# Kernel tuning notes

Hardware: AMD Instinct MI355X
Metric: run time of the kernel (lower is better)

## Reference

```python
import jax, jax.numpy as jnp
import numpy as np

V = 50257
VPAD = 50304
D = 768
H = 6
HD = 128
L = 12
T = 2048
BLOCK = 128
NB = T // BLOCK
EPS = 1.1920929e-07  # torch.finfo(float32).eps, F.rms_norm default
ATTN_SCALE = 0.12


def rms_norm(x):
    return x * jax.lax.rsqrt(jnp.mean(jnp.square(x), axis=-1, keepdims=True) + EPS)


def rotary_tables(t):
    af = (1.0 / 1024) ** jnp.linspace(0.0, 1.0, HD // 4)
    af = jnp.concatenate([af, jnp.zeros(HD // 4)])  # half of HD/2 freqs are zero
    theta = jnp.arange(t, dtype=jnp.float32)[:, None] * af[None, :]  # [T, HD/2]
    return jnp.cos(theta), jnp.sin(theta)


def apply_rotary(x, cos, sin):
    # x: [B,T,H,HD]
    x1, x2 = jnp.split(x, 2, axis=-1)
    c = cos[None, :, None, :]
    s = sin[None, :, None, :]
    return jnp.concatenate([x1 * c + x2 * s, -x1 * s + x2 * c], axis=-1)


def build_elem_masks(input_seq, sw_long):
    # Reproduces create_block_masks: block-sparse document-causal + sliding window.
    docs = jnp.cumsum((input_seq == 50256).astype(jnp.int32))
    bi = jnp.arange(NB)
    docs_b = docs.reshape(NB, BLOCK)
    dlo, dhi = docs_b[:, 0], docs_b[:, -1]
    any_bm = (bi[:, None] >= bi[None, :]) & (dlo[:, None] <= dhi[None, :]) & (dhi[:, None] >= dlo[None, :])
    all_bm = (bi[:, None] > bi[None, :]) & (dlo[:, None] == dhi[None, :]) & (dhi[:, None] == dlo[None, :])
    partial_bm = any_bm & (~all_bm)

    def rank_desc(m):
        # rank of each True block among that row's True blocks ordered by descending kv index
        mi = m.astype(jnp.int32)
        return jnp.cumsum(mi[:, ::-1], axis=1)[:, ::-1] - mi

    pr = rank_desc(partial_bm)
    fr = rank_desc(all_bm)
    full_cnt = jnp.sum(all_bm.astype(jnp.int32), axis=1)
    ti = jnp.arange(T)
    causal_e = ti[:, None] >= ti[None, :]
    doc_e = docs[:, None] == docs[None, :]

    def bm(sw):
        # BlockMask.from_kv_blocks keeps nearest blocks:
        # partial kept count = min(partial_cnt, max(sw - full_cnt, 1)); full kept count = min(full_cnt, sw - 1)
        keep_p = partial_bm & (pr < jnp.maximum(sw - full_cnt, 1)[:, None])
        keep_f = all_bm & (fr < (sw - 1))
        kp = jnp.repeat(jnp.repeat(keep_p, BLOCK, axis=0), BLOCK, axis=1)
        kf = jnp.repeat(jnp.repeat(keep_f, BLOCK, axis=0), BLOCK, axis=1)
        # full blocks skip mask_mod; partial blocks apply elementwise document_causal
        return kf | (kp & causal_e & doc_e)

    return bm(sw_long), bm(sw_long // 2)


def attention(x, ve, qkv_w, lam, proj_w, cos, sin, mask):
    B = x.shape[0]
    qkv = jnp.einsum('btd,fd->btf', x, qkv_w.reshape(3 * H * HD, D))
    q, k, v = [a.reshape(B, T, H, HD) for a in jnp.split(qkv, 3, axis=-1)]
    q = apply_rotary(rms_norm(q), cos, sin)
    k = apply_rotary(rms_norm(k), cos, sin)
    if ve is not None:
        v = lam[0] * v + lam[1] * ve.reshape(v.shape)
    else:
        v = lam[0] * v
    scores = jnp.einsum('bthd,bshd->bhts', q, k) * ATTN_SCALE
    scores = jnp.where(mask[None, None], scores, -jnp.inf)
    p = jax.nn.softmax(scores, axis=-1)
    y = jnp.einsum('bhts,bshd->bthd', p, v).reshape(B, T, H * HD)
    return y @ proj_w.T


def mlp(x, fc_w, proj_w):
    h = x @ fc_w.T
    return jnp.square(jax.nn.relu(h)) @ proj_w.T


def forward(input_seq, target_seq, sw, embed_w, ve_w, qkv_w, attn_lambdas, attn_proj_w,
            mlp_fc_w, mlp_proj_w, block_lambdas, skip_weights, lm_head_w):
    long_m, short_m = build_elem_masks(input_seq, sw)
    cos, sin = rotary_tables(T)
    x = x0 = rms_norm(embed_w[input_seq][None])  # [1,T,D]
    ve0, ve1, ve2 = ve_w[0][input_seq], ve_w[1][input_seq], ve_w[2][input_seq]
    ve = [ve0, ve1, ve2, None, None, None, None, None, None, ve0, ve1, ve2]
    enc_masks = [long_m, short_m, short_m, short_m, long_m, short_m]
    masks = enc_masks + enc_masks[::-1]
    skips = []
    for i in range(6):  # encoder
        x = block_lambdas[i, 0] * x + block_lambdas[i, 1] * x0
        x = x + attention(rms_norm(x), ve[i], qkv_w[i], attn_lambdas[i], attn_proj_w[i], cos, sin, masks[i])
        x = x + mlp(rms_norm(x), mlp_fc_w[i], mlp_proj_w[i])
        skips.append(x)
    for j in range(6):  # decoder with U-net skips
        i = 6 + j
        x = x + skip_weights[j] * skips.pop()
        x = block_lambdas[i, 0] * x + block_lambdas[i, 1] * x0
        if i != 7:  # layer 7 has no attention
            x = x + attention(rms_norm(x), ve[i], qkv_w[i], attn_lambdas[i], attn_proj_w[i], cos, sin, masks[i])
        x = x + mlp(rms_norm(x), mlp_fc_w[i], mlp_proj_w[i])
    x = rms_norm(x)
    logits = (x @ lm_head_w.T).astype(jnp.float32)
    logits = 30.0 * jax.nn.sigmoid(logits / (7.5 * (D ** 0.5)))
    logp = jax.nn.log_softmax(logits.reshape(T, VPAD), axis=-1)
    return -jnp.mean(jnp.take_along_axis(logp, target_seq[:, None], axis=1))


def setup_inputs():
    key = jax.random.key(0)
    ks = jax.random.split(key, 10)

    def rn(k, shape, std):
        return jax.random.normal(k, shape, dtype=jnp.float32) * std

    s_d = 0.5 / (D ** 0.5)
    s_h = 0.5 / ((4 * D) ** 0.5)
    input_seq = jax.random.randint(ks[0], (T,), 0, V)
    input_seq = input_seq.at[jnp.arange(0, T, 512)].set(50256)  # doc separators
    return {
        'input_seq': input_seq,
        'target_seq': jax.random.randint(ks[1], (T,), 0, V),
        'sliding_window_num_blocks': 8,
        'embed_w': rn(ks[2], (V, D), 0.02),
        've_w': rn(ks[3], (3, V, D), 0.02),
        'qkv_w': rn(ks[4], (L, 3, H * HD, D), s_d),
        'attn_lambdas': jnp.tile(jnp.array([0.5, 0.5], dtype=jnp.float32), (L, 1)),
        'attn_proj_w': rn(ks[5], (L, D, H * HD), s_d),
        'mlp_fc_w': rn(ks[6], (L, 4 * D, D), s_d),
        'mlp_proj_w': rn(ks[7], (L, D, 4 * D), s_h),
        'block_lambdas': jnp.tile(jnp.array([1.0, 0.0], dtype=jnp.float32), (L, 1)),
        'skip_weights': jnp.ones((6,), dtype=jnp.float32),
        'lm_head_w': rn(ks[8], (VPAD, D), 0.005),
    }


def reference(input_seq, target_seq, sliding_window_num_blocks, embed_w, ve_w, qkv_w,
              attn_lambdas, attn_proj_w, mlp_fc_w, mlp_proj_w, block_lambdas,
              skip_weights, lm_head_w):
    return forward(input_seq, target_seq, sliding_window_num_blocks, embed_w, ve_w, qkv_w,
                   attn_lambdas, attn_proj_w, mlp_fc_w, mlp_proj_w, block_lambdas,
                   skip_weights, lm_head_w)
```

## Files before the change

### kernel.cpp

```cpp
#include <hip/hip_runtime.h>
#include <hip/hip_bf16.h>

#define TT 2048
#define DD 768
#define HH 6
#define HDIM 128
#define NL 12
#define NBL 16
#define BLKSZ 128
#define DFF 3072
#define VP 50304
#define NV 50257
#define EPSF 1.1920929e-07f

typedef unsigned short u16;
typedef __attribute__((ext_vector_type(8))) short short8v;
typedef __attribute__((ext_vector_type(4))) float f32x4;
typedef __attribute__((address_space(3))) void lds_void;
typedef __attribute__((address_space(1))) void gbl_void;

__device__ __forceinline__ u16 f2bf(float f){
  unsigned u = __float_as_uint(f);
  return (u16)((u + 0x7fffu + ((u >> 16) & 1u)) >> 16);
}
__device__ __forceinline__ float bf2f(u16 u){
  return __uint_as_float((unsigned)u << 16);
}
__device__ __forceinline__ void async16(const void* g, void* l){
  __builtin_amdgcn_global_load_lds((const gbl_void*)g, (lds_void*)l, 16, 0, 0);
}

__device__ __forceinline__ float wave_sum(float v){
#pragma unroll
  for (int o = 32; o > 0; o >>= 1) v += __shfl_xor(v, o);
  return v;
}
__device__ __forceinline__ float block_sum(float v){
  __shared__ float sh[9];
  int lane = threadIdx.x & 63, w = threadIdx.x >> 6;
  v = wave_sum(v);
  if (lane == 0) sh[w] = v;
  __syncthreads();
  if (threadIdx.x == 0){
    float tot = 0.f;
    int nw = (blockDim.x + 63) >> 6;
    for (int i = 0; i < nw; i++) tot += sh[i];
    sh[8] = tot;
  }
  __syncthreads();
  return sh[8];
}

__global__ void k_f2bf_all(const float* __restrict__ qkvw, const float* __restrict__ aproj,
                           const float* __restrict__ fcw, const float* __restrict__ mproj,
                           const float* __restrict__ lmw,
                           u16* __restrict__ qkvw_bf, u16* __restrict__ aprojw_bf,
                           u16* __restrict__ fcw_bf, u16* __restrict__ mprojw_bf,
                           u16* __restrict__ lmw_bf){
  const long S0 = 2654208;
  const long S1 = S0 + 884736;
  const long S2 = S1 + 3538944;
  const long S3 = S2 + 3538944;
  const long S4 = S3 + 4829184;
  long stride = (long)gridDim.x * blockDim.x;
  for (long g = (long)blockIdx.x * blockDim.x + threadIdx.x; g < S4; g += stride){
    const float* in; u16* out; long off;
    if (g < S0){ in = qkvw;  out = qkvw_bf;  off = g; }
    else if (g < S1){ in = aproj; out = aprojw_bf; off = g - S0; }
    else if (g < S2){ in = fcw;   out = fcw_bf;   off = g - S1; }
    else if (g < S3){ in = mproj; out = mprojw_bf; off = g - S2; }
    else { in = lmw; out = lmw_bf; off = g - S3; }
    const float4* p = (const float4*)(in + off * 8);
    float4 a = p[0], b = p[1];
    u16 o[8] = { f2bf(a.x), f2bf(a.y), f2bf(a.z), f2bf(a.w),
                 f2bf(b.x), f2bf(b.y), f2bf(b.z), f2bf(b.w) };
    *(ulonglong2*)(out + off * 8) = *(const ulonglong2*)o;
  }
}

__global__ void k_docs_masks(const int* __restrict__ seq, const int* __restrict__ swnb,
                             int* __restrict__ docs, int* __restrict__ bmask){
  int lane = threadIdx.x;
  int cnt = 0;
  for (int i = 0; i < 32; i++) cnt += (seq[lane*32 + i] == 50256);
  int incl = cnt;
#pragma unroll
  for (int o = 1; o < 64; o <<= 1){
    int v = __shfl_up(incl, o);
    if (lane >= o) incl += v;
  }
  int run = incl - cnt;
  for (int i = 0; i < 32; i++){
    int t = lane*32 + i;
    run += (seq[t] == 50256);
    docs[t] = run;
  }
  __syncthreads();
  if (lane != 0) return;
  int dlo[NBL], dhi[NBL];
  for (int b = 0; b < NBL; b++){ dlo[b] = docs[b*BLKSZ]; dhi[b] = docs[b*BLKSZ + BLKSZ-1]; }
  int allb[NBL][NBL], partb[NBL][NBL];
  for (int i = 0; i < NBL; i++)
    for (int j = 0; j < NBL; j++){
      int a = (i >= j) && (dlo[i] <= dhi[j]) && (dhi[i] >= dlo[j]);
      int f = (i >  j) && (dlo[i] == dhi[j]) && (dhi[i] == dlo[j]);
      allb[i][j] = f; partb[i][j] = a && !f;
    }
  int sws[2]; sws[0] = swnb[0]; sws[1] = swnb[0] / 2;
  for (int m = 0; m < 2; m++){
    int sw = sws[m];
    for (int i = 0; i < NBL; i++){
      int fullcnt = 0;
      for (int j = 0; j < NBL; j++) fullcnt += allb[i][j];
      int pth = sw - fullcnt; if (pth < 1) pth = 1;
      int pr = 0, fr = 0;
      for (int j = NBL-1; j >= 0; j--){
        int kp = partb[i][j] && (pr < pth);
        int kf = allb[i][j]  && (fr < sw - 1);
        bmask[(m*2+0)*NBL*NBL + i*NBL + j] = kf;
        bmask[(m*2+1)*NBL*NBL + i*NBL + j] = kp;
        pr += partb[i][j]; fr += allb[i][j];
      }
    }
  }
}

__global__ void k_embed(const int* __restrict__ seq, const float* __restrict__ embw,
                        const float* __restrict__ vew, float* __restrict__ x,
                        float* __restrict__ x0, u16* __restrict__ veg,
                        float* __restrict__ cosb, float* __restrict__ sinb){
  int t = blockIdx.x;
  if (threadIdx.x < 64){
    int j = threadIdx.x;
    float c = 1.f, s = 0.f;
    if (j < 32){
      float af = powf(1.0f/1024.0f, (float)j / 31.0f);
      float th = (float)t * af;
      c = cosf(th); s = sinf(th);
    }
    cosb[t*64 + j] = c; sinb[t*64 + j] = s;
  }
  int tok = seq[t];
  const float* row = embw + (size_t)tok * DD;
  float ss = 0.f;
  for (int d = threadIdx.x; d < DD; d += blockDim.x){ float v = row[d]; ss += v*v; }
  float tot = block_sum(ss);
  float rn = rsqrtf(tot / DD + EPSF);
  for (int d = threadIdx.x; d < DD; d += blockDim.x){
    float v = row[d] * rn;
    x[(size_t)t*DD + d] = v; x0[(size_t)t*DD + d] = v;
  }
  for (int j = 0; j < 3; j++){
    const float* vr = vew + ((size_t)j*NV + tok) * DD;
    u16* dst = veg + ((size_t)j*TT + t) * DD;
    for (int d = threadIdx.x; d < DD; d += blockDim.x) dst[d] = f2bf(vr[d]);
  }
}

__global__ void k_rmsnorm_bf(const float* __restrict__ in, u16* __restrict__ out,
                             float* __restrict__ rowsum){
  int t = blockIdx.x;
  if (rowsum && threadIdx.x == 0) rowsum[t] = 0.f;
  const float* r = in + (size_t)t * DD;
  float ss = 0.f;
  for (int d = threadIdx.x; d < DD; d += blockDim.x){ float v = r[d]; ss += v*v; }
  float tot = block_sum(ss);
  float rn = rsqrtf(tot / DD + EPSF);
  u16* o = out + (size_t)t * DD;
  for (int d = threadIdx.x; d < DD; d += blockDim.x) o[d] = f2bf(r[d] * rn);
}

__global__ void k_premix_norm(float* __restrict__ x, const float* __restrict__ x0,
                              const float* __restrict__ sk, float* __restrict__ sk_out,
                              const float* __restrict__ skw, int j,
                              const float* __restrict__ bl, int layer, u16* __restrict__ xn){
  int t = blockIdx.x;
  float bl0 = bl[layer*2], bl1 = bl[layer*2 + 1];
  float sw = sk ? skw[j] : 0.f;
  float vloc[3];
  float ss = 0.f;
  int base = t * DD;
#pragma unroll
  for (int k = 0; k < 3; k++){
    int d = threadIdx.x + k*256;
    float xin = x[base + d];
    if (sk_out) sk_out[base + d] = xin;
    float v = xin;
    if (sk) v += sw * sk[base + d];
    v = bl0 * v + bl1 * x0[base + d];
    vloc[k] = v; ss += v*v;
  }
  float tot = block_sum(ss);
  float rn = rsqrtf(tot / DD + EPSF);
#pragma unroll
  for (int k = 0; k < 3; k++){
    int d = threadIdx.x + k*256;
    x[base + d] = vloc[k];
    xn[base + d] = f2bf(vloc[k] * rn);
  }
}

template<int MODE, int BN>
__global__ __launch_bounds__(256, (BN == 64) ? 3 : 2)
void k_mfma_gemm(const u16* __restrict__ A, const u16* __restrict__ B,
                 float* __restrict__ C, u16* __restrict__ Cbf,
                 const u16* __restrict__ vegp, const float* __restrict__ lam,
                 int layer, u16* __restrict__ vtb,
                 const float* __restrict__ cosb, const float* __restrict__ sinb,
                 u16* __restrict__ qbf, u16* __restrict__ kbf,
                 int N, int K, int ldk, int nbn){
  constexpr int NW   = BN / 32;
  constexpr int BC   = BN / 32;
  constexpr int NBUF = (BN == 64) ? 2 : 1;
  __shared__ u16 As[NBUF][128*64];
  __shared__ u16 Bs[NBUF][BN*64];
  __shared__ float qt[(MODE == 4) ? 32*132 : 1];
  int per = (nbn << 4) >> 3;
  int x = (blockIdx.x & 7) * per + (blockIdx.x >> 3);
  int bm = (x & 15) << 7;
  int bn = (x >> 4) * BN;
  int koff = (MODE == 5) ? blockIdx.y * K : 0;
  int tid = threadIdx.x;
  int wid = tid >> 6, lane = tid & 63;
  int wr = wid >> 1, wc = wid & 1;
  int srow = lane >> 3;
  int scol = (((lane & 7) ^ srow) * 8);
  int l15 = lane & 15, l16 = lane >> 4;
  const u16* pa[4];
  const u16* pb[BC];
#pragma unroll
  for (int c = 0; c < 4; c++){
    int row = (wid*4 + c)*8 + srow;
    pa[c] = A + (size_t)(bm + row) * ldk + koff + scol;
  }
#pragma unroll
  for (int c = 0; c < BC; c++){
    int row = (wid*BC + c)*8 + srow;
    pb[c] = B + (size_t)(bn + row) * ldk + koff + scol;
  }
  f32x4 acc[4][NW] = {};
  auto stage = [&](int buf){
#pragma unroll
    for (int c = 0; c < 4; c++){
      async16(pa[c], &As[buf][(wid*4 + c) * 512]);
      pa[c] += 64;
    }
#pragma unroll
    for (int c = 0; c < BC; c++){
      async16(pb[c], &Bs[buf][(wid*BC + c) * 512]);
      pb[c] += 64;
    }
  };
  auto compute = [&](int buf){
#pragma unroll
    for (int kk = 0; kk < 2; kk++){
      short8v a[4], b[NW];
#pragma unroll
      for (int m = 0; m < 4; m++){
        int row = wr*64 + m*16 + l15;
        a[m] = *(const short8v*)(&As[buf][row*64 + ((((kk<<2)|l16) ^ (row&7))<<3)]);
      }
#pragma unroll
      for (int n = 0; n < NW; n++){
        int row = wc*(BN/2) + n*16 + l15;
        b[n] = *(const short8v*)(&Bs[buf][row*64 + ((((kk<<2)|l16) ^ (row&7))<<3)]);
      }
#pragma unroll
      for (int m = 0; m < 4; m++)
#pragma unroll
        for (int n = 0; n < NW; n++)
          acc[m][n] = __builtin_amdgcn_mfma_f32_16x16x32_bf16(a[m], b[n], acc[m][n], 0, 0, 0);
    }
  };
  if constexpr (BN == 64){
    stage(0);
    int KT = K >> 6;
    for (int t = 0; t < KT; t++){
      int cur = t & 1;
      if (t + 1 < KT){
        stage(cur ^ 1);
        asm volatile("s_waitcnt vmcnt(6)" ::: "memory");
      } else {
        asm volatile("s_waitcnt vmcnt(0)" ::: "memory");
      }
      __builtin_amdgcn_s_barrier();
      asm volatile("" ::: "memory");
      compute(cur);
      asm volatile("" ::: "memory");
      __builtin_amdgcn_s_barrier();
    }
  } else {
    for (int k0 = 0; k0 < K; k0 += 64){
      stage(0);
      __syncthreads();
      compute(0);
      __syncthreads();
    }
  }
  if (MODE == 4){
    if (bn >= 1536){
      int h = (bn - 1536) >> 7;
      float l0 = lam[layer*2], l1 = lam[layer*2 + 1];
#pragma unroll
      for (int m = 0; m < 4; m++){
        int t0 = bm + wr*64 + m*16 + l16*4;
#pragma unroll
        for (int n = 0; n < NW; n++){
          int d = wc*64 + n*16 + l15;
          u16 o[4];
#pragma unroll
          for (int j = 0; j < 4; j++){
            float v = l0 * acc[m][n][j];
            if (vegp) v += l1 * bf2f(vegp[(size_t)(t0 + j)*DD + h*HDIM + d]);
            o[j] = f2bf(v);
          }
          *(ushort4*)(vtb + ((size_t)(h*HDIM + d))*TT + t0) = *(const ushort4*)o;
        }
      }
    } else {
      int h = (bn < 768) ? (bn >> 7) : ((bn - 768) >> 7);
      u16* dstb = (bn < 768) ? qbf : kbf;
#pragma unroll
      for (int p = 0; p < 4; p++){
        if (wr == (p >> 1)){
#pragma unroll
          for (int mm = 0; mm < 2; mm++){
            int m = (p & 1)*2 + mm;
#pragma unroll
            for (int n = 0; n < NW; n++){
              int col = wc*64 + n*16 + l15;
#pragma unroll
              for (int j = 0; j < 4; j++){
                int lr = m*16 + l16*4 + j - (p & 1)*32;
                qt[lr*132 + col] = acc[m][n][j];
              }
            }
          }
        }
        __syncthreads();
        {
          int row = tid >> 3, part = tid & 7;
          int tok = bm + p*32 + row;
          float ss = 0.f;
#pragma unroll
          for (int jj = 0; jj < 16; jj++){
            float v = qt[row*132 + part*16 + jj];
            ss += v*v;
          }
          ss += __shfl_xor(ss, 1); ss += __shfl_xor(ss, 2); ss += __shfl_xor(ss, 4);
          float rn = rsqrtf(ss / 128.f + EPSF);
          if (part < 4){
            u16* dst = dstb + ((size_t)(h*TT + tok))*HDIM;
#pragma unroll
            for (int jj = 0; jj < 16; jj++){
              int j = part*16 + jj;
              float c = cosb[tok*64 + j], s = sinb[tok*64 + j];
              float v1 = qt[row*132 + j] * rn;
              float v2 = qt[row*132 + j + 64] * rn;
              dst[j]      = f2bf(v1*c + v2*s);
              dst[j + 64] = f2bf(-v1*s + v2*c);
            }
          }
        }
        __syncthreads();
      }
    }
    return;
  }
#pragma unroll
  for (int m = 0; m < 4; m++){
    int row = bm + wr*64 + m*16 + l16*4;
#pragma unroll
    for (int j = 0; j < 4; j++){
      if (MODE == 3){
        u16* cb = Cbf + (size_t)(row + j) * N + bn + wc*(BN/2) + l15;
#pragma unroll
        for (int n = 0; n < NW; n++){
          float v = fmaxf(acc[m][n][j], 0.f);
          cb[n*16] = f2bf(v * v);
        }
      } else if (MODE == 5){
        float* cp = C + (size_t)(row + j) * N + bn + wc*(BN/2) + l15;
#pragma unroll
        for (int n = 0; n < NW; n++) atomicAdd(cp + n*16, acc[m][n][j]);
      } else {
        float* cp = C + (size_t)(row + j) * N + bn + wc*(BN/2) + l15;
#pragma unroll
        for (int n = 0; n < NW; n++) cp[n*16] = acc[m][n][j];
      }
    }
  }
}

__global__ __launch_bounds__(256) void k_loss_mfma(const u16* __restrict__ A, const u16* __restrict__ B,
                                                   const int* __restrict__ tgt, float* __restrict__ rowsum,
                                                   float* __restrict__ tl){
  __shared__ u16 As[128*64];
  __shared__ u16 Bs[128*64];
  const int nbn = VP/128;
  int per = (nbn << 4) >> 3;
  int x = (blockIdx.x & 7) * per + (blockIdx.x >> 3);
  int bm = (x & 15) << 7;
  int bn = (x >> 4) << 7;
  int tid = threadIdx.x;
  int wid = tid >> 6, lane = tid & 63;
  int wr = wid >> 1, wc = wid & 1;
  int srow = lane >> 3;
  int scol = (((lane & 7) ^ srow) * 8);
  int l15 = lane & 15, l16 = lane >> 4;
  const u16* pa[4];
  const u16* pb[4];
#pragma unroll
  for (int c = 0; c < 4; c++){
    int row = (wid*4 + c)*8 + srow;
    pa[c] = A + (size_t)(bm + row) * DD + scol;
    pb[c] = B + (size_t)(bn + row) * DD + scol;
  }
  f32x4 acc[4][4] = {};
  for (int k0 = 0; k0 < DD; k0 += 64){
#pragma unroll
    for (int c = 0; c < 4; c++){
      int chunk = wid * 4 + c;
      async16(pa[c], As + chunk * 512);
      async16(pb[c], Bs + chunk * 512);
      pa[c] += 64; pb[c] += 64;
    }
    __syncthreads();
#pragma unroll
    for (int kk = 0; kk < 2; kk++){
      short8v a[4], b[4];
#pragma unroll
      for (int m = 0; m < 4; m++)
        a[m] = *(const short8v*)(As + (wr*64 + m*16 + l15)*64 + ((((kk<<2)|l16) ^ (l15&7))<<3));
#pragma unroll
      for (int n = 0; n < 4; n++)
        b[n] = *(const short8v*)(Bs + (wc*64 + n*16 + l15)*64 + ((((kk<<2)|l16) ^ (l15&7))<<3));
#pragma unroll
      for (int m = 0; m < 4; m++)
#pragma unroll
        for (int n = 0; n < 4; n++)
          acc[m][n] = __builtin_amdgcn_mfma_f32_16x16x32_bf16(a[m], b[n], acc[m][n], 0, 0, 0);
    }
    __syncthreads();
  }
  const float INVS = 0.0048112522432469f;
#pragma unroll
  for (int m = 0; m < 4; m++){
#pragma unroll
    for (int j = 0; j < 4; j++){
      int row = bm + wr*64 + m*16 + l16*4 + j;
      int tg = tgt[row];
      float rs = 0.f;
#pragma unroll
      for (int n = 0; n < 4; n++){
        int col = bn + wc*64 + n*16 + l15;
        float lg = 30.f * __builtin_amdgcn_rcpf(1.f + __expf(-acc[m][n][j] * INVS));
        rs += __expf(lg);
        if (col == tg) tl[row] = lg;
      }
      rs += __shfl_xor(rs, 1); rs += __shfl_xor(rs, 2);
      rs += __shfl_xor(rs, 4); rs += __shfl_xor(rs, 8);
      if (l15 == 0) atomicAdd(&rowsum[row], rs);
    }
  }
}

__global__ __launch_bounds__(256) void k_attn_mfma(
    const u16* __restrict__ qbf, const u16* __restrict__ kbf, const u16* __restrict__ vtb,
    u16* __restrict__ y, const int* __restrict__ docs,
    const int* __restrict__ kfm, const int* __restrict__ kpm){
  __shared__ u16 Ks[128*128];
  __shared__ u16 Vs[128*128];
  __shared__ int docsL[128];
  __shared__ int kb[NBL], kfl[NBL];
  __shared__ int nkb_sh;
  int wg = (blockIdx.x & 7) * 24 + (blockIdx.x >> 3);
  int h = wg >> 5;
  int qb = (31 - (wg & 31)) * 64;
  int bt = qb >> 7;
  int tid = threadIdx.x;
  int w = tid >> 6, lane = tid & 63;
  int l15 = lane & 15, l16 = lane >> 4;
  if (tid == 0){
    int n = 0;
    for (int sb = 0; sb <= bt; sb++){
      int kf = kfm[bt*NBL + sb], kp = kpm[bt*NBL + sb];
      if (kf || kp){ kb[n] = sb; kfl[n] = kf; n++; }
    }
    nkb_sh = n;
  }
  short8v q[4];
  {
    const u16* qrow = qbf + ((size_t)(h*TT + qb + w*16 + l15))*HDIM;
#pragma unroll
    for (int kc = 0; kc < 4; kc++) q[kc] = *(const short8v*)(qrow + kc*32 + l16*8);
  }
  int t_row[4], dq[4];
#pragma unroll
  for (int j = 0; j < 4; j++){
    t_row[j] = qb + w*16 + l16*4 + j;
    dq[j] = docs[t_row[j]];
  }
  f32x4 o[8] = {};
  float m[4], l[4];
#pragma unroll
  for (int j = 0; j < 4; j++){ m[j] = -1e30f; l[j] = 0.f; }
  __syncthreads();
  int nkb = nkb_sh;
  for (int bi = 0; bi < nkb; bi++){
    int kbi = kb[bi], kf = kfl[bi];
    __syncthreads();
    {
      const u16* ksrc = kbf + ((size_t)(h*TT + kbi*128))*HDIM;
      const u16* vsrc = vtb + ((size_t)(h*HDIM))*TT + kbi*128;
#pragma unroll
      for (int p = 0; p < 8; p++){
        int idx = tid + p*256;
        int r = idx >> 4, c = (idx & 15) * 8;
        short8v kv = *(const short8v*)(ksrc + (size_t)r*HDIM + c);
        *(short8v*)(Ks + ((r*128 + c) ^ ((r&7)<<3))) = kv;
        short8v vv = *(const short8v*)(vsrc + (size_t)r*TT + c);
        *(short8v*)(Vs + ((r*128 + c) ^ ((r&7)<<3))) = vv;
      }
      if (tid < 32) ((int4*)docsL)[tid] = ((const int4*)(docs + kbi*128))[tid];
    }
    __syncthreads();
    f32x4 s[8];
#pragma unroll
    for (int n = 0; n < 8; n++){
      f32x4 acc = {};
#pragma unroll
      for (int kc = 0; kc < 4; kc++){
        int row = n*16 + l15;
        short8v b = *(const short8v*)(Ks + ((row*128 + kc*32 + l16*8) ^ ((row&7)<<3)));
        acc = __builtin_amdgcn_mfma_f32_16x16x32_bf16(q[kc], b, acc, 0, 0, 0);
      }
      s[n] = acc;
    }
    int sbase = kbi*128;
    float bmax[4];
#pragma unroll
    for (int j = 0; j < 4; j++) bmax[j] = -1e30f;
#pragma unroll
    for (int n = 0; n < 8; n++){
      int sg = sbase + n*16 + l15;
      int ds = docsL[n*16 + l15];
#pragma unroll
      for (int j = 0; j < 4; j++){
        float sv = s[n][j] * 0.12f;
        bool keep = kf || ((sg <= t_row[j]) && (ds == dq[j]));
        sv = keep ? sv : -1e30f;
        s[n][j] = sv;
        bmax[j] = fmaxf(bmax[j], sv);
      }
    }
#pragma unroll
    for (int j = 0; j < 4; j++){
#pragma unroll
      for (int off = 1; off < 16; off <<= 1) bmax[j] = fmaxf(bmax[j], __shfl_xor(bmax[j], off));
      float nm = fmaxf(m[j], bmax[j]);
      float r = __expf(m[j] - nm);
      m[j] = nm; l[j] *= r;
#pragma unroll
      for (int n = 0; n < 8; n++) o[n][j] *= r;
    }
    __syncthreads();
#pragma unroll
    for (int n = 0; n < 8; n++){
#pragma unroll
      for (int j = 0; j < 4; j++){
        float sv = s[n][j];
        float p = (sv > -1e29f) ? __expf(sv - m[j]) : 0.f;
        l[j] += p;
        int prow = w*16 + l16*4 + j;
        Ks[((prow*128) + n*16 + l15) ^ ((prow&7)<<3)] = f2bf(p);
      }
    }
    __syncthreads();
    short8v a[4];
    {
      int prow = w*16 + l15;
#pragma unroll
      for (int kc = 0; kc < 4; kc++)
        a[kc] = *(const short8v*)(Ks + ((prow*128 + kc*32 + l16*8) ^ ((prow&7)<<3)));
    }
#pragma unroll
    for (int n = 0; n < 8; n++){
#pragma unroll
      for (int kc = 0; kc < 4; kc++){
        int vrow = n*16 + l15;
        short8v b = *(const short8v*)(Vs + ((vrow*128 + kc*32 + l16*8) ^ ((vrow&7)<<3)));
        o[n] = __builtin_amdgcn_mfma_f32_16x16x32_bf16(a[kc], b, o[n], 0, 0, 0);
      }
    }
  }
  float inv[4];
#pragma unroll
  for (int j = 0; j < 4; j++){
    float lt = l[j];
#pragma unroll
    for (int off = 1; off < 16; off <<= 1) lt += __shfl_xor(lt, off);
    inv[j] = 1.f / lt;
  }
#pragma unroll
  for (int n = 0; n < 8; n++){
#pragma unroll
    for (int j = 0; j < 4; j++)
      y[(size_t)t_row[j]*DD + h*HDIM + n*16 + l15] = f2bf(o[n][j] * inv[j]);
  }
}

__global__ void k_loss_final(const float* __restrict__ rowsum, const float* __restrict__ tl,
                             float* __restrict__ out){
  float a = 0.f;
  for (int t = threadIdx.x; t < TT; t += 256) a += logf(rowsum[t]) - tl[t];
  a = block_sum(a);
  if (threadIdx.x == 0) out[0] = a / TT;
}

extern "C" void kernel_launch(void* const* d_in, const int* in_sizes, int n_in,
                              void* d_out, int out_size, void* d_ws, size_t ws_size,
                              hipStream_t stream){
  const int*   seq   = (const int*)d_in[0];
  const int*   tgt   = (const int*)d_in[1];
  const int*   swnb  = (const int*)d_in[2];
  const float* embw  = (const float*)d_in[3];
  const float* vew   = (const float*)d_in[4];
  const float* qkvw  = (const float*)d_in[5];
  const float* alam  = (const float*)d_in[6];
  const float* aproj = (const float*)d_in[7];
  const float* fcw   = (const float*)d_in[8];
  const float* mproj = (const float*)d_in[9];
  const float* blam  = (const float*)d_in[10];
  const float* skw   = (const float*)d_in[11];
  const float* lmw   = (const float*)d_in[12];

  char* base = (char*)d_ws;
  size_t off = 0;
  auto alloc = [&](size_t bytes){ char* p = base + off; off += (bytes + 255) & ~(size_t)255; return p; };
  float* x     = (float*)alloc((size_t)TT*DD*4);
  float* x0    = (float*)alloc((size_t)TT*DD*4);
  float* skips = (float*)alloc((size_t)5*TT*DD*4);
  float* cosb  = (float*)alloc((size_t)TT*64*4);
  float* sinb  = (float*)alloc((size_t)TT*64*4);
  float* rowsum= (float*)alloc(TT*4);
  float* tl    = (float*)alloc(TT*4);
  int* docs    = (int*)alloc(TT*4);
  int* bmask   = (int*)alloc(4*NBL*NBL*4);
  u16* veg     = (u16*)alloc((size_t)3*TT*DD*2);
  u16* xn_bf   = (u16*)alloc((size_t)TT*DD*2);
  u16* y_bf    = (u16*)alloc((size_t)TT*DD*2);
  u16* hb_bf   = (u16*)alloc((size_t)TT*DFF*2);
  u16* qbf     = (u16*)alloc((size_t)HH*TT*HDIM*2);
  u16* kbf     = (u16*)alloc((size_t)HH*TT*HDIM*2);
  u16* vtb     = (u16*)alloc((size_t)HH*HDIM*TT*2);
  u16* qkvw_bf = (u16*)alloc((size_t)NL*2304*DD*2);
  u16* aprojw_bf = (u16*)alloc((size_t)NL*DD*DD*2);
  u16* fcw_bf  = (u16*)alloc((size_t)NL*DFF*DD*2);
  u16* mprojw_bf = (u16*)alloc((size_t)NL*DD*DFF*2);
  u16* lmw_bf  = (u16*)alloc((size_t)VP*DD*2);

  k_f2bf_all<<<4096, 256, 0, stream>>>(qkvw, aproj, fcw, mproj, lmw,
                                       qkvw_bf, aprojw_bf, fcw_bf, mprojw_bf, lmw_bf);
  k_docs_masks<<<1, 64, 0, stream>>>(seq, swnb, docs, bmask);
  k_embed<<<TT, 256, 0, stream>>>(seq, embw, vew, x, x0, veg, cosb, sinb);

  static const int msel[12] = {0,1,1,1,0,1, 1,0,1,1,1,0};
  for (int i = 0; i < NL; i++){
    const float* sk = nullptr;
    if (i == 6) sk = x;
    else if (i > 6) sk = skips + (size_t)(11 - i)*TT*DD;
    float* sk_out = (i >= 1 && i <= 5) ? (skips + (size_t)(i - 1)*TT*DD) : nullptr;
    k_premix_norm<<<TT, 256, 0, stream>>>(x, x0, sk, sk_out, skw, i - 6, blam, i, xn_bf);
    if (i != 7){
      const u16* vp = nullptr;
      if (i < 3) vp = veg + (size_t)i*TT*DD;
      else if (i >= 9) vp = veg + (size_t)(i - 9)*TT*DD;
      k_mfma_gemm<4,128><<<16*18, 256, 0, stream>>>(xn_bf, qkvw_bf + (size_t)i*2304*DD, nullptr,
                                                    nullptr, vp, alam, i, vtb, cosb, sinb, qbf, kbf,
                                                    2304, DD, DD, 18);
      const int* kfm = bmask + (msel[i]*2 + 0)*NBL*NBL;
      const int* kpm = bmask + (msel[i]*2 + 1)*NBL*NBL;
      k_attn_mfma<<<192, 256, 0, stream>>>(qbf, kbf, vtb, y_bf, docs, kfm, kpm);
      dim3 gap(16*12, 2);
      k_mfma_gemm<5,64><<<gap, 256, 0, stream>>>(y_bf, aprojw_bf + (size_t)i*DD*DD, x,
                                                 nullptr, nullptr, nullptr, 0, nullptr,
                                                 nullptr, nullptr, nullptr, nullptr, DD, 384, DD, 12);
      k_rmsnorm_bf<<<TT, 256, 0, stream>>>(x, xn_bf, nullptr);
    }
    k_mfma_gemm<3,64><<<16*48, 256, 0, stream>>>(xn_bf, fcw_bf + (size_t)i*DFF*DD, nullptr,
                                                 hb_bf, nullptr, nullptr, 0, nullptr,
                                                 nullptr, nullptr, nullptr, nullptr, DFF, DD, DD, 48);
    dim3 gmp(16*12, 4);
    k_mfma_gemm<5,64><<<gmp, 256, 0, stream>>>(hb_bf, mprojw_bf + (size_t)i*DD*DFF, x,
                                               nullptr, nullptr, nullptr, 0, nullptr,
                                               nullptr, nullptr, nullptr, nullptr, DD, 768, DFF, 12);
  }
  k_rmsnorm_bf<<<TT, 256, 0, stream>>>(x, xn_bf, rowsum);
  k_loss_mfma<<<16*(VP/128), 256, 0, stream>>>(xn_bf, lmw_bf, tgt, rowsum, tl);
  k_loss_final<<<1, 256, 0, stream>>>(rowsum, tl, (float*)d_out);
}
```

Baseline: 2.163 ms.

## Double-buffer LDS tiles in loss GEMM to overlap async loads with MFMA

The fused lm_head/loss kernel now keeps two LDS buffers for the A and B tiles. It issues the async global-to-LDS loads for the next K tile before computing the current one, and uses an explicit vmcnt wait plus barriers in place of the full __syncthreads. The goal is to hide global load latency behind MFMA work. It also raises wave priority around the compute. LDS use per block doubles to 64KB, which may reduce occupancy.

```diff
diff --git a/kernel.cpp b/kernel.cpp
--- a/kernel.cpp
+++ b/kernel.cpp
@@ -395,8 +395,8 @@
 __global__ __launch_bounds__(256) void k_loss_mfma(const u16* __restrict__ A, const u16* __restrict__ B,
                                                    const int* __restrict__ tgt, float* __restrict__ rowsum,
                                                    float* __restrict__ tl){
-  __shared__ u16 As[128*64];
-  __shared__ u16 Bs[128*64];
+  __shared__ u16 As[2][128*64];
+  __shared__ u16 Bs[2][128*64];
   const int nbn = VP/128;
   int per = (nbn << 4) >> 3;
   int x = (blockIdx.x & 7) * per + (blockIdx.x >> 3);
@@ -417,31 +417,52 @@
     pb[c] = B + (size_t)(bn + row) * DD + scol;
   }
   f32x4 acc[4][4] = {};
-  for (int k0 = 0; k0 < DD; k0 += 64){
+  auto stage = [&](int buf){
 #pragma unroll
     for (int c = 0; c < 4; c++){
-      int chunk = wid * 4 + c;
-      async16(pa[c], As + chunk * 512);
-      async16(pb[c], Bs + chunk * 512);
+      async16(pa[c], &As[buf][(wid*4 + c) * 512]);
+      async16(pb[c], &Bs[buf][(wid*4 + c) * 512]);
       pa[c] += 64; pb[c] += 64;
     }
-    __syncthreads();
+  };
+  auto compute = [&](int buf){
 #pragma unroll
     for (int kk = 0; kk < 2; kk++){
       short8v a[4], b[4];
 #pragma unroll
-      for (int m = 0; m < 4; m++)
-        a[m] = *(const short8v*)(As + (wr*64 + m*16 + l15)*64 + ((((kk<<2)|l16) ^ (l15&7))<<3));
-#pragma unroll
-      for (int n = 0; n < 4; n++)
-        b[n] = *(const short8v*)(Bs + (wc*64 + n*16 + l15)*64 + ((((kk<<2)|l16) ^ (l15&7))<<3));
+      for (int m = 0; m < 4; m++){
+        int row = wr*64 + m*16 + l15;
+        a[m] = *(const short8v*)(&As[buf][row*64 + ((((kk<<2)|l16) ^ (row&7))<<3)]);
+      }
+#pragma unroll
+      for (int n = 0; n < 4; n++){
+        int row = wc*64 + n*16 + l15;
+        b[n] = *(const short8v*)(&Bs[buf][row*64 + ((((kk<<2)|l16) ^ (row&7))<<3)]);
+      }
 #pragma unroll
       for (int m = 0; m < 4; m++)
 #pragma unroll
         for (int n = 0; n < 4; n++)
           acc[m][n] = __builtin_amdgcn_mfma_f32_16x16x32_bf16(a[m], b[n], acc[m][n], 0, 0, 0);
     }
-    __syncthreads();
+  };
+  stage(0);
+  const int KT = DD >> 6;
+  for (int t = 0; t < KT; t++){
+    int cur = t & 1;
+    if (t + 1 < KT){
+      stage(cur ^ 1);
+      asm volatile("s_waitcnt vmcnt(8)" ::: "memory");
+    } else {
+      asm volatile("s_waitcnt vmcnt(0)" ::: "memory");
+    }
+    __builtin_amdgcn_s_barrier();
+    asm volatile("" ::: "memory");
+    __builtin_amdgcn_s_setprio(1);
+    compute(cur);
+    __builtin_amdgcn_s_setprio(0);
+    asm volatile("" ::: "memory");
+    __builtin_amdgcn_s_barrier();
   }
   const float INVS = 0.0048112522432469f;
 #pragma unroll
```

New measurement: 2.157 ms, median of 2. About the same (-0.3%).
